# Performance work log

Measured on AMD Instinct MI355X. Metric: run time of the kernel, lower is better.

## Reference

```python
import jax, jax.numpy as jnp
import numpy as np

N = 8192  # n_nodes
E = 262144  # edges per adjacency (avg degree 32)


def setup_inputs() -> dict:
    key = jax.random.key(0)
    k0, k1, k2, k3, k4, k5 = jax.random.split(key, 6)
    rows_s = jax.random.randint(k0, (E,), 0, N)
    cols_s = jax.random.randint(k1, (E,), 0, N)
    vals_s = jax.random.uniform(k2, (E,), dtype=jnp.float32)
    rows_t = jax.random.randint(k3, (E,), 0, N)
    cols_t = jax.random.randint(k4, (E,), 0, N)
    vals_t = jax.random.uniform(k5, (E,), dtype=jnp.float32)
    gamma = jnp.zeros((1,), dtype=jnp.float32)  # learnable scalar, init 0.0
    return {
        "rows_s": rows_s, "cols_s": cols_s, "vals_s": vals_s,
        "rows_t": rows_t, "cols_t": cols_t, "vals_t": vals_t,
        "gamma": gamma,
    }


def reference(rows_s, cols_s, vals_s, rows_t, cols_t, vals_t, gamma):
    # coalesce + to_dense: scatter-add duplicates into dense [N, N]
    As = jnp.zeros((N, N), dtype=vals_s.dtype).at[rows_s, cols_s].add(vals_s)
    At = jnp.zeros((N, N), dtype=vals_t.dtype).at[rows_t, cols_t].add(vals_t)
    alpha = jax.nn.sigmoid(gamma[0])
    Af = alpha * As + (1.0 - alpha) * At
    row_sum = jnp.sum(Af, axis=1, keepdims=True)  # [N, 1]
    row_sum = jnp.where(row_sum == 0, jnp.ones_like(row_sum), row_sum)
    Af = Af / row_sum
    # torch returns Af.to_sparse(); dense Af is the equivalent value-complete output
    return Af
```

## Files before the change

### kernel.cpp

```cpp
#include <hip/hip_runtime.h>
#include <math.h>

#define NN 8192
#define NE 262144

__global__ __launch_bounds__(256) void rowsum_kernel(
        const int* __restrict__ rows_s, const float* __restrict__ vals_s,
        const int* __restrict__ rows_t, const float* __restrict__ vals_t,
        const float* __restrict__ gamma, float* __restrict__ row_sum) {
    int i = blockIdx.x * blockDim.x + threadIdx.x;
    float alpha = 1.0f / (1.0f + expf(-gamma[0]));
    if (i < NE) {
        atomicAdd(&row_sum[rows_s[i]], alpha * vals_s[i]);
    } else {
        int j = i - NE;
        atomicAdd(&row_sum[rows_t[j]], (1.0f - alpha) * vals_t[j]);
    }
}

__global__ __launch_bounds__(256) void scatter_kernel(
        const int* __restrict__ rows_s, const int* __restrict__ cols_s,
        const float* __restrict__ vals_s,
        const int* __restrict__ rows_t, const int* __restrict__ cols_t,
        const float* __restrict__ vals_t,
        const float* __restrict__ gamma, const float* __restrict__ row_sum,
        float* __restrict__ out) {
    int i = blockIdx.x * blockDim.x + threadIdx.x;
    float alpha = 1.0f / (1.0f + expf(-gamma[0]));
    int r, c;
    float v, w;
    if (i < NE) {
        r = rows_s[i]; c = cols_s[i]; v = vals_s[i]; w = alpha;
    } else {
        int j = i - NE;
        r = rows_t[j]; c = cols_t[j]; v = vals_t[j]; w = 1.0f - alpha;
    }
    float s = row_sum[r];
    if (s == 0.0f) s = 1.0f;
    atomicAdd(&out[(size_t)r * NN + c], (w * v) / s);
}

extern "C" void kernel_launch(void* const* d_in, const int* in_sizes, int n_in,
                              void* d_out, int out_size, void* d_ws, size_t ws_size,
                              hipStream_t stream) {
    const int*   rows_s = (const int*)  d_in[0];
    const int*   cols_s = (const int*)  d_in[1];
    const float* vals_s = (const float*)d_in[2];
    const int*   rows_t = (const int*)  d_in[3];
    const int*   cols_t = (const int*)  d_in[4];
    const float* vals_t = (const float*)d_in[5];
    const float* gamma  = (const float*)d_in[6];

    float* out     = (float*)d_out;
    float* row_sum = (float*)d_ws;

    hipMemsetAsync(d_out, 0, (size_t)NN * NN * sizeof(float), stream);
    hipMemsetAsync(d_ws, 0, (size_t)NN * sizeof(float), stream);

    const int total = 2 * NE;
    const int block = 256;
    const int grid  = total / block;

    rowsum_kernel<<<grid, block, 0, stream>>>(rows_s, vals_s, rows_t, vals_t,
                                              gamma, row_sum);
    scatter_kernel<<<grid, block, 0, stream>>>(rows_s, cols_s, vals_s,
                                               rows_t, cols_t, vals_t,
                                               gamma, row_sum, out);
}
```

Measured before the change: 336.9 us.

## Bucket edges by row via counting sort, build rows in LDS

Replaces global-atomic scatter into a memset output with a CSR-style bucketing pass (count, scan, fill) followed by a per-row kernel that accumulates the row in shared memory, normalizes it, and writes it out with coalesced float4 stores. This removes the separate full-matrix memset and the scattered global atomics on the 256 MB output, so each output element is written exactly once. The cost is three extra small kernels, a single-block scan, and extra workspace traffic for the bucketed columns and values. Summation order within a row is now nondeterministic in shared memory rather than in global memory.

```diff
diff --git a/kernel.cpp b/kernel.cpp
--- a/kernel.cpp
+++ b/kernel.cpp
@@ -3,41 +3,104 @@
 
 #define NN 8192
 #define NE 262144
+#define TOTAL (2*NE)
 
-__global__ __launch_bounds__(256) void rowsum_kernel(
-        const int* __restrict__ rows_s, const float* __restrict__ vals_s,
-        const int* __restrict__ rows_t, const float* __restrict__ vals_t,
-        const float* __restrict__ gamma, float* __restrict__ row_sum) {
+#define WS_OFF    8192
+#define WS_CUR    16640
+#define WS_BCOL   24832
+#define WS_BVAL   (24832 + TOTAL)
+
+__global__ __launch_bounds__(256) void count_kernel(
+        const int* __restrict__ rows_s, const int* __restrict__ rows_t,
+        int* __restrict__ cnt) {
     int i = blockIdx.x * blockDim.x + threadIdx.x;
-    float alpha = 1.0f / (1.0f + expf(-gamma[0]));
-    if (i < NE) {
-        atomicAdd(&row_sum[rows_s[i]], alpha * vals_s[i]);
-    } else {
-        int j = i - NE;
-        atomicAdd(&row_sum[rows_t[j]], (1.0f - alpha) * vals_t[j]);
-    }
+    int r = (i < NE) ? rows_s[i] : rows_t[i - NE];
+    atomicAdd(&cnt[r], 1);
 }
 
-__global__ __launch_bounds__(256) void scatter_kernel(
+__global__ __launch_bounds__(1024) void scan_kernel(
+        const int* __restrict__ cnt, int* __restrict__ off, int* __restrict__ cursor) {
+    __shared__ int sums[1024];
+    int t = threadIdx.x;
+    int base = t * 8;
+    int local[8];
+    int s = 0;
+    #pragma unroll
+    for (int k = 0; k < 8; k++) { local[k] = s; s += cnt[base + k]; }
+    sums[t] = s;
+    __syncthreads();
+    for (int d = 1; d < 1024; d <<= 1) {
+        int v = (t >= d) ? sums[t - d] : 0;
+        __syncthreads();
+        sums[t] += v;
+        __syncthreads();
+    }
+    int prefix = (t == 0) ? 0 : sums[t - 1];
+    #pragma unroll
+    for (int k = 0; k < 8; k++) {
+        int o = prefix + local[k];
+        off[base + k]    = o;
+        cursor[base + k] = o;
+    }
+    if (t == 1023) off[NN] = sums[1023];
+}
+
+__global__ __launch_bounds__(256) void fill_kernel(
         const int* __restrict__ rows_s, const int* __restrict__ cols_s,
         const float* __restrict__ vals_s,
         const int* __restrict__ rows_t, const int* __restrict__ cols_t,
         const float* __restrict__ vals_t,
-        const float* __restrict__ gamma, const float* __restrict__ row_sum,
-        float* __restrict__ out) {
+        const float* __restrict__ gamma,
+        int* __restrict__ cursor, int* __restrict__ bcol, float* __restrict__ bval) {
     int i = blockIdx.x * blockDim.x + threadIdx.x;
     float alpha = 1.0f / (1.0f + expf(-gamma[0]));
-    int r, c;
-    float v, w;
-    if (i < NE) {
-        r = rows_s[i]; c = cols_s[i]; v = vals_s[i]; w = alpha;
-    } else {
-        int j = i - NE;
-        r = rows_t[j]; c = cols_t[j]; v = vals_t[j]; w = 1.0f - alpha;
+    int r, c; float v, w;
+    if (i < NE) { r = rows_s[i]; c = cols_s[i]; v = vals_s[i]; w = alpha; }
+    else { int j = i - NE; r = rows_t[j]; c = cols_t[j]; v = vals_t[j]; w = 1.0f - alpha; }
+    int pos = atomicAdd(&cursor[r], 1);
+    bcol[pos] = c;
+    bval[pos] = w * v;
+}
+
+__global__ __launch_bounds__(256) void row_kernel(
+        const int* __restrict__ off,
+        const int* __restrict__ bcol, const float* __restrict__ bval,
+        float* __restrict__ out) {
+    __shared__ float row[NN];
+    __shared__ float red[4];
+    int r = blockIdx.x;
+    int t = threadIdx.x;
+
+    #pragma unroll 8
+    for (int k = t; k < NN; k += 256) row[k] = 0.0f;
+    __syncthreads();
+
+    int start = off[r], end = off[r + 1];
+    for (int k = start + t; k < end; k += 256)
+        atomicAdd(&row[bcol[k]], bval[k]);
+    __syncthreads();
+
+    float s = 0.0f;
+    #pragma unroll 8
+    for (int k = t; k < NN; k += 256) s += row[k];
+    #pragma unroll
+    for (int o = 32; o > 0; o >>= 1) s += __shfl_down(s, o, 64);
+    int wave = t >> 6, lane = t & 63;
+    if (lane == 0) red[wave] = s;
+    __syncthreads();
+    float total = red[0] + red[1] + red[2] + red[3];
+    float inv = (total == 0.0f) ? 1.0f : 1.0f / total;
+
+    float4* out4 = (float4*)(out + (size_t)r * NN);
+    #pragma unroll 2
+    for (int k = t; k < NN / 4; k += 256) {
+        float4 x;
+        x.x = row[4 * k + 0] * inv;
+        x.y = row[4 * k + 1] * inv;
+        x.z = row[4 * k + 2] * inv;
+        x.w = row[4 * k + 3] * inv;
+        out4[k] = x;
     }
-    float s = row_sum[r];
-    if (s == 0.0f) s = 1.0f;
-    atomicAdd(&out[(size_t)r * NN + c], (w * v) / s);
 }
 
 extern "C" void kernel_launch(void* const* d_in, const int* in_sizes, int n_in,
@@ -51,19 +114,20 @@
     const float* vals_t = (const float*)d_in[5];
     const float* gamma  = (const float*)d_in[6];
 
-    float* out     = (float*)d_out;
-    float* row_sum = (float*)d_ws;
+    float* out    = (float*)d_out;
+    int*   ws     = (int*)d_ws;
+    int*   cnt    = ws;
+    int*   off    = ws + WS_OFF;
+    int*   cursor = ws + WS_CUR;
+    int*   bcol   = ws + WS_BCOL;
+    float* bval   = (float*)(ws + WS_BVAL);
 
-    hipMemsetAsync(d_out, 0, (size_t)NN * NN * sizeof(float), stream);
-    hipMemsetAsync(d_ws, 0, (size_t)NN * sizeof(float), stream);
+    hipMemsetAsync(cnt, 0, NN * sizeof(int), stream);
 
-    const int total = 2 * NE;
-    const int block = 256;
-    const int grid  = total / block;
-
-    rowsum_kernel<<<grid, block, 0, stream>>>(rows_s, vals_s, rows_t, vals_t,
-                                              gamma, row_sum);
-    scatter_kernel<<<grid, block, 0, stream>>>(rows_s, cols_s, vals_s,
-                                               rows_t, cols_t, vals_t,
-                                               gamma, row_sum, out);
+    count_kernel<<<TOTAL / 256, 256, 0, stream>>>(rows_s, rows_t, cnt);
+    scan_kernel<<<1, 1024, 0, stream>>>(cnt, off, cursor);
+    fill_kernel<<<TOTAL / 256, 256, 0, stream>>>(rows_s, cols_s, vals_s,
+                                                 rows_t, cols_t, vals_t,
+                                                 gamma, cursor, bcol, bval);
+    row_kernel<<<NN, 256, 0, stream>>>(off, bcol, bval, out);
 }
```

Measured after the change: 335.5 us. Within noise of the previous version (-0.4%).

## Bucket edges per row, then build and normalize each dense row in LDS

Applied to the files above, without the earlier changes.

Replaces the global memset, global atomic row-sum and global atomic scatter with two stages. First, edges are binned into fixed-capacity per-row buckets, with an overflow list for rows that exceed the capacity. Then one block per row accumulates the row in shared memory, reduces the row sum, and writes the normalized row with nontemporal vector stores. This removes the separate 256MB zeroing pass and the scattered global atomics, at the cost of every block scanning the whole overflow list when overflow is nonzero.

```diff
diff --git a/kernel.cpp b/kernel.cpp
--- a/kernel.cpp
+++ b/kernel.cpp
@@ -3,41 +3,92 @@
 
 #define NN 8192
 #define NE 262144
+#define TOTAL (2*NE)
+#define CAP 128
 
-__global__ __launch_bounds__(256) void rowsum_kernel(
-        const int* __restrict__ rows_s, const float* __restrict__ vals_s,
-        const int* __restrict__ rows_t, const float* __restrict__ vals_t,
-        const float* __restrict__ gamma, float* __restrict__ row_sum) {
-    int i = blockIdx.x * blockDim.x + threadIdx.x;
-    float alpha = 1.0f / (1.0f + expf(-gamma[0]));
-    if (i < NE) {
-        atomicAdd(&row_sum[rows_s[i]], alpha * vals_s[i]);
-    } else {
-        int j = i - NE;
-        atomicAdd(&row_sum[rows_t[j]], (1.0f - alpha) * vals_t[j]);
-    }
-}
+typedef float f4 __attribute__((ext_vector_type(4)));
 
-__global__ __launch_bounds__(256) void scatter_kernel(
+struct Pair { int c; float v; };
+
+#define BK_OFF (65536)
+#define OV_OFF (65536 + (size_t)NN * CAP * 8)
+
+__global__ __launch_bounds__(256) void fill_kernel(
         const int* __restrict__ rows_s, const int* __restrict__ cols_s,
         const float* __restrict__ vals_s,
         const int* __restrict__ rows_t, const int* __restrict__ cols_t,
         const float* __restrict__ vals_t,
-        const float* __restrict__ gamma, const float* __restrict__ row_sum,
-        float* __restrict__ out) {
+        const float* __restrict__ gamma,
+        int* __restrict__ cnt, Pair* __restrict__ bucket,
+        int* __restrict__ ovf_cnt, int4* __restrict__ ovf) {
     int i = blockIdx.x * blockDim.x + threadIdx.x;
     float alpha = 1.0f / (1.0f + expf(-gamma[0]));
-    int r, c;
-    float v, w;
-    if (i < NE) {
-        r = rows_s[i]; c = cols_s[i]; v = vals_s[i]; w = alpha;
+    int r, c; float v, w;
+    if (i < NE) { r = rows_s[i]; c = cols_s[i]; v = vals_s[i]; w = alpha; }
+    else { int j = i - NE; r = rows_t[j]; c = cols_t[j]; v = vals_t[j]; w = 1.0f - alpha; }
+    float wv = w * v;
+    int pos = atomicAdd(&cnt[r], 1);
+    if (pos < CAP) {
+        Pair p; p.c = c; p.v = wv;
+        bucket[r * CAP + pos] = p;
     } else {
-        int j = i - NE;
-        r = rows_t[j]; c = cols_t[j]; v = vals_t[j]; w = 1.0f - alpha;
+        int k = atomicAdd(ovf_cnt, 1);
+        int4 e; e.x = r; e.y = c; e.z = __float_as_int(wv); e.w = 0;
+        ovf[k] = e;
     }
-    float s = row_sum[r];
-    if (s == 0.0f) s = 1.0f;
-    atomicAdd(&out[(size_t)r * NN + c], (w * v) / s);
+}
+
+__global__ __launch_bounds__(256) void row_kernel(
+        const int* __restrict__ cnt, const Pair* __restrict__ bucket,
+        const int* __restrict__ ovf_cnt, const int4* __restrict__ ovf,
+        float* __restrict__ out) {
+    __shared__ float row[NN];
+    __shared__ float red[4];
+    int r = blockIdx.x;
+    int t = threadIdx.x;
+
+    f4* row4 = (f4*)row;
+    #pragma unroll
+    for (int k = t; k < NN / 4; k += 256) {
+        f4 z = {0.f, 0.f, 0.f, 0.f};
+        row4[k] = z;
+    }
+    int n = cnt[r];
+    int nb = n < CAP ? n : CAP;
+    __syncthreads();
+
+    float part = 0.0f;
+    for (int k = t; k < nb; k += 256) {
+        Pair p = bucket[r * CAP + k];
+        part += p.v;
+        atomicAdd(&row[p.c], p.v);
+    }
+    int no = *ovf_cnt;
+    if (no > 0) {
+        for (int k = t; k < no; k += 256) {
+            int4 e = ovf[k];
+            if (e.x == r) {
+                float v = __int_as_float(e.z);
+                part += v;
+                atomicAdd(&row[e.y], v);
+            }
+        }
+    }
+
+    #pragma unroll
+    for (int o = 32; o > 0; o >>= 1) part += __shfl_down(part, o, 64);
+    if ((t & 63) == 0) red[t >> 6] = part;
+    __syncthreads();
+    float total = red[0] + red[1] + red[2] + red[3];
+    float inv = (total == 0.0f) ? 1.0f : 1.0f / total;
+
+    f4* out4 = (f4*)(out + (size_t)r * NN);
+    #pragma unroll
+    for (int k = t; k < NN / 4; k += 256) {
+        f4 x = row4[k];
+        x *= inv;
+        __builtin_nontemporal_store(x, &out4[k]);
+    }
 }
 
 extern "C" void kernel_launch(void* const* d_in, const int* in_sizes, int n_in,
@@ -52,18 +103,16 @@
     const float* gamma  = (const float*)d_in[6];
 
     float* out     = (float*)d_out;
-    float* row_sum = (float*)d_ws;
+    char*  ws      = (char*)d_ws;
+    int*   cnt     = (int*)ws;
+    int*   ovf_cnt = (int*)(ws + 32768);
+    Pair*  bucket  = (Pair*)(ws + BK_OFF);
+    int4*  ovf     = (int4*)(ws + OV_OFF);
 
-    hipMemsetAsync(d_out, 0, (size_t)NN * NN * sizeof(float), stream);
-    hipMemsetAsync(d_ws, 0, (size_t)NN * sizeof(float), stream);
+    (void)hipMemsetAsync(ws, 0, 32772, stream);
 
-    const int total = 2 * NE;
-    const int block = 256;
-    const int grid  = total / block;
-
-    rowsum_kernel<<<grid, block, 0, stream>>>(rows_s, vals_s, rows_t, vals_t,
-                                              gamma, row_sum);
-    scatter_kernel<<<grid, block, 0, stream>>>(rows_s, cols_s, vals_s,
-                                               rows_t, cols_t, vals_t,
-                                               gamma, row_sum, out);
+    fill_kernel<<<TOTAL / 256, 256, 0, stream>>>(rows_s, cols_s, vals_s,
+                                                 rows_t, cols_t, vals_t,
+                                                 gamma, cnt, bucket, ovf_cnt, ovf);
+    row_kernel<<<NN, 256, 0, stream>>>(cnt, bucket, ovf_cnt, ovf, out);
 }
```

After: 308.9 us. 8.3% less time.
